# Performance work log

Hardware: AMD Instinct MI355X
Metric: run time of the kernel (lower is better)

Reference implementation:

```python
import jax, jax.numpy as jnp
import numpy as np

# Token / dim constants (from vm_step.Token and vm_step._SetDim)
CODE_START, CODE_END, MEM = 256, 257, 258
ADDR_KEY, MEM_STORE = 206, 455
VOCAB, D_MODEL = 272, 512
B, S = 16, 8192


def setup_inputs() -> dict:
    key = jax.random.key(0)
    k1, k2 = jax.random.split(key)
    token_ids = jax.random.randint(k1, (B, S), 0, VOCAB)
    embed_weight = jax.random.normal(k2, (VOCAB, D_MODEL), dtype=jnp.float32) * 0.02
    return {"token_ids": token_ids, "embed_weight": embed_weight, "mem_history_end": 2048}


def _augment_mask(token_ids, mem_history_end):
    """Boolean [B, S, D_MODEL] mask of positions that get set to 1.0."""
    Bb, Ss = token_ids.shape
    idx = jnp.arange(Ss)                                  # [S]
    is_start = token_ids == CODE_START
    is_end = token_ids == CODE_END
    # loop breaks at the FIRST CODE_END in each row
    end_idx = jnp.min(jnp.where(is_end, idx[None, :], Ss), axis=1)      # [B]
    # cs_pos = index of most recent CODE_START at-or-before i (-1 if none)
    cs = jax.lax.cummax(jnp.where(is_start, idx[None, :], -1), axis=1)  # [B,S]
    addr = idx[None, :] - cs - 1                                        # [B,S]
    valid = (cs >= 0) & (idx[None, :] < end_idx[:, None]) \
            & (token_ids < 256) & (addr >= 0)
    lo = addr & 15
    hi = (addr >> 4) & 15
    top = (addr >> 8) & 15
    bins = jnp.arange(16)                                 # nibble one-hots
    lo_oh = (bins == lo[..., None]) & valid[..., None]    # [B,S,16]
    hi_oh = (bins == hi[..., None]) & valid[..., None]
    top_oh = (bins == top[..., None]) & valid[..., None]
    mem_flag = (token_ids == MEM) & (idx[None, :] < mem_history_end)    # [B,S]

    mask = jnp.zeros((Bb, Ss, D_MODEL), dtype=bool)
    mask = mask.at[:, :, ADDR_KEY:ADDR_KEY + 16].set(lo_oh)
    mask = mask.at[:, :, ADDR_KEY + 16:ADDR_KEY + 32].set(hi_oh)
    mask = mask.at[:, :, ADDR_KEY + 32:ADDR_KEY + 48].set(top_oh)
    mask = mask.at[:, :, MEM_STORE].set(mem_flag)
    return mask


def reference(token_ids, embed_weight, mem_history_end):
    x = embed_weight[token_ids]                           # [B,S,D] gather
    mask = _augment_mask(token_ids, mem_history_end)
    return jnp.where(mask, jnp.asarray(1.0, x.dtype), x)
```

## Files before the change

### kernel.cpp

```cpp
#include <hip/hip_runtime.h>

#define TOK_CODE_START 256
#define TOK_CODE_END   257
#define TOK_MEM        258
#define ADDR_KEY       206
#define MEM_STORE      455

constexpr int Bb = 16;
constexpr int Ss = 8192;
constexpr int DM = 512;

typedef float f32x4 __attribute__((ext_vector_type(4)));

__global__ __launch_bounds__(1024) void vm_scan_kernel(
    const int* __restrict__ tok,
    const int* __restrict__ mhe_p,
    unsigned int* __restrict__ ws)
{
    const int b = blockIdx.x;
    const int t = threadIdx.x;
    const int lane = t & 63;
    const int wid = t >> 6;
    const int mhe = mhe_p[0];
    const int* row = tok + b * Ss;
    const int base = t * 8;

    int toks[8];
    int4 v0 = reinterpret_cast<const int4*>(row + base)[0];
    int4 v1 = reinterpret_cast<const int4*>(row + base)[1];
    toks[0] = v0.x; toks[1] = v0.y; toks[2] = v0.z; toks[3] = v0.w;
    toks[4] = v1.x; toks[5] = v1.y; toks[6] = v1.z; toks[7] = v1.w;

    int lmax = -1;
    int lend = Ss;
    #pragma unroll
    for (int k = 0; k < 8; ++k) {
        int idx = base + k;
        if (toks[k] == TOK_CODE_START) lmax = idx;
        if (toks[k] == TOK_CODE_END && lend == Ss) lend = idx;
    }

    #pragma unroll
    for (int off = 1; off < 64; off <<= 1) {
        int u = __shfl_up(lmax, off);
        if (lane >= off && u > lmax) lmax = u;
    }
    int excl = __shfl_up(lmax, 1);
    if (lane == 0) excl = -1;

    #pragma unroll
    for (int off = 32; off > 0; off >>= 1) {
        int u = __shfl_xor(lend, off);
        if (u < lend) lend = u;
    }

    __shared__ int wmax[16];
    __shared__ int wend[16];
    if (lane == 63) wmax[wid] = lmax;
    if (lane == 0)  wend[wid] = lend;
    __syncthreads();

    int carry = -1;
    #pragma unroll
    for (int j = 0; j < 16; ++j)
        if (j < wid && wmax[j] > carry) carry = wmax[j];
    int end_idx = Ss;
    #pragma unroll
    for (int j = 0; j < 16; ++j)
        if (wend[j] < end_idx) end_idx = wend[j];

    int run = (carry > excl) ? carry : excl;

    unsigned int pk[8];
    #pragma unroll
    for (int k = 0; k < 8; ++k) {
        int idx = base + k;
        int tv = toks[k];
        if (tv == TOK_CODE_START) run = idx;
        int cs = run;
        int addr = idx - cs - 1;
        bool valid = (cs >= 0) && (idx < end_idx) && (tv < 256) && (addr >= 0);
        bool memf  = (tv == TOK_MEM) && (idx < mhe);
        unsigned int w = (unsigned int)tv;
        if (valid) w |= (1u << 9) | ((unsigned int)addr << 11);
        if (memf)  w |= (1u << 10);
        pk[k] = w;
    }
    uint4* wr = reinterpret_cast<uint4*>(ws + b * Ss + base);
    wr[0] = make_uint4(pk[0], pk[1], pk[2], pk[3]);
    wr[1] = make_uint4(pk[4], pk[5], pk[6], pk[7]);
}

__global__ __launch_bounds__(256) void vm_gather_kernel(
    const f32x4* __restrict__ emb,
    const unsigned int* __restrict__ ws,
    f32x4* __restrict__ out)
{
    const int total = Bb * Ss * (DM / 4);
    const int stride = gridDim.x * blockDim.x;
    for (int w = blockIdx.x * blockDim.x + threadIdx.x; w < total; w += stride) {
        int bs = w >> 7;
        int dq = w & 127;
        unsigned int pw = ws[bs];
        int tk = (int)(pw & 511u);
        f32x4 v = emb[tk * (DM / 4) + dq];
        unsigned int flags = pw >> 9;
        if (flags) {
            bool valid = (flags & 1u) != 0u;
            bool memf  = (flags & 2u) != 0u;
            int addr = (int)(flags >> 2);
            int p0 = ADDR_KEY      + (addr & 15);
            int p1 = ADDR_KEY + 16 + ((addr >> 4) & 15);
            int p2 = ADDR_KEY + 32 + ((addr >> 8) & 15);
            int d0 = dq << 2;
            #pragma unroll
            for (int j = 0; j < 4; ++j) {
                int d = d0 + j;
                if ((valid && (d == p0 || d == p1 || d == p2)) ||
                    (memf && d == MEM_STORE)) v[j] = 1.0f;
            }
        }
        __builtin_nontemporal_store(v, &out[w]);
    }
}

extern "C" void kernel_launch(void* const* d_in, const int* in_sizes, int n_in,
                              void* d_out, int out_size, void* d_ws, size_t ws_size,
                              hipStream_t stream) {
    const int* tok = (const int*)d_in[0];
    const float* emb = (const float*)d_in[1];
    const int* mhe = (const int*)d_in[2];
    unsigned int* ws = (unsigned int*)d_ws;
    f32x4* out = (f32x4*)d_out;

    vm_scan_kernel<<<Bb, 1024, 0, stream>>>(tok, mhe, ws);
    vm_gather_kernel<<<2048, 256, 0, stream>>>((const f32x4*)emb, ws, out);
}
```

Before: 51.43 us.

## Fuse token scan and embedding gather into one kernel with per-block prefix rescan

```diff
diff --git a/kernel.cpp b/kernel.cpp
--- a/kernel.cpp
+++ b/kernel.cpp
@@ -9,101 +9,101 @@
 constexpr int Bb = 16;
 constexpr int Ss = 8192;
 constexpr int DM = 512;
+constexpr int POS_PER_BLK = 64;
+constexpr int QPP = DM / 4;
+constexpr int THREADS = 256;
 
 typedef float f32x4 __attribute__((ext_vector_type(4)));
 
-__global__ __launch_bounds__(1024) void vm_scan_kernel(
+__global__ __launch_bounds__(THREADS) void vm_fused_kernel(
     const int* __restrict__ tok,
+    const f32x4* __restrict__ emb,
     const int* __restrict__ mhe_p,
-    unsigned int* __restrict__ ws)
+    f32x4* __restrict__ out)
 {
-    const int b = blockIdx.x;
-    const int t = threadIdx.x;
+    const int bk = blockIdx.x;
+    const int b  = bk >> 7;
+    const int c  = bk & 127;
+    const int t  = threadIdx.x;
     const int lane = t & 63;
-    const int wid = t >> 6;
+    const int wid  = t >> 6;
+    const int s0 = c * POS_PER_BLK;
+    const int* row = tok + b * Ss;
     const int mhe = mhe_p[0];
-    const int* row = tok + b * Ss;
-    const int base = t * 8;
 
-    int toks[8];
-    int4 v0 = reinterpret_cast<const int4*>(row + base)[0];
-    int4 v1 = reinterpret_cast<const int4*>(row + base)[1];
-    toks[0] = v0.x; toks[1] = v0.y; toks[2] = v0.z; toks[3] = v0.w;
-    toks[4] = v1.x; toks[5] = v1.y; toks[6] = v1.z; toks[7] = v1.w;
+    __shared__ int sP[4], sE[4];
+    __shared__ unsigned int smask[POS_PER_BLK];
 
-    int lmax = -1;
-    int lend = Ss;
-    #pragma unroll
-    for (int k = 0; k < 8; ++k) {
-        int idx = base + k;
-        if (toks[k] == TOK_CODE_START) lmax = idx;
-        if (toks[k] == TOK_CODE_END && lend == Ss) lend = idx;
+    int myTok = 0;
+    if (t < POS_PER_BLK) myTok = row[s0 + t];
+
+    int maxStart = -1;
+    int minEnd = Ss;
+    {
+        const int base = t * 32;
+        if (base < s0) {
+            #pragma unroll
+            for (int j = 0; j < 8; ++j) {
+                int4 v = reinterpret_cast<const int4*>(row + base + j * 4)[0];
+                int i0 = base + j * 4;
+                if (v.x == TOK_CODE_START) maxStart = i0;
+                if (v.y == TOK_CODE_START) maxStart = i0 + 1;
+                if (v.z == TOK_CODE_START) maxStart = i0 + 2;
+                if (v.w == TOK_CODE_START) maxStart = i0 + 3;
+                if (v.x == TOK_CODE_END && minEnd == Ss) minEnd = i0;
+                if (v.y == TOK_CODE_END && minEnd == Ss) minEnd = i0 + 1;
+                if (v.z == TOK_CODE_END && minEnd == Ss) minEnd = i0 + 2;
+                if (v.w == TOK_CODE_END && minEnd == Ss) minEnd = i0 + 3;
+            }
+        }
     }
-
-    #pragma unroll
-    for (int off = 1; off < 64; off <<= 1) {
-        int u = __shfl_up(lmax, off);
-        if (lane >= off && u > lmax) lmax = u;
-    }
-    int excl = __shfl_up(lmax, 1);
-    if (lane == 0) excl = -1;
-
     #pragma unroll
     for (int off = 32; off > 0; off >>= 1) {
-        int u = __shfl_xor(lend, off);
-        if (u < lend) lend = u;
+        int u = __shfl_xor(maxStart, off);
+        if (u > maxStart) maxStart = u;
+        int w = __shfl_xor(minEnd, off);
+        if (w < minEnd) minEnd = w;
     }
-
-    __shared__ int wmax[16];
-    __shared__ int wend[16];
-    if (lane == 63) wmax[wid] = lmax;
-    if (lane == 0)  wend[wid] = lend;
+    if (lane == 0) { sP[wid] = maxStart; sE[wid] = minEnd; }
     __syncthreads();
 
-    int carry = -1;
-    #pragma unroll
-    for (int j = 0; j < 16; ++j)
-        if (j < wid && wmax[j] > carry) carry = wmax[j];
-    int end_idx = Ss;
-    #pragma unroll
-    for (int j = 0; j < 16; ++j)
-        if (wend[j] < end_idx) end_idx = wend[j];
+    if (t < POS_PER_BLK) {
+        int P = max(max(sP[0], sP[1]), max(sP[2], sP[3]));
+        int E = min(min(sE[0], sE[1]), min(sE[2], sE[3]));
 
-    int run = (carry > excl) ? carry : excl;
-
-    unsigned int pk[8];
-    #pragma unroll
-    for (int k = 0; k < 8; ++k) {
-        int idx = base + k;
-        int tv = toks[k];
-        if (tv == TOK_CODE_START) run = idx;
-        int cs = run;
+        const int idx = s0 + t;
+        int st = (myTok == TOK_CODE_START) ? idx : -1;
+        int en = (myTok == TOK_CODE_END) ? idx : Ss;
+        #pragma unroll
+        for (int off = 1; off < 64; off <<= 1) {
+            int u = __shfl_up(st, off);
+            int v = __shfl_up(en, off);
+            if (lane >= off) {
+                if (u > st) st = u;
+                if (v < en) en = v;
+            }
+        }
+        int cs = max(P, st);
+        int firstEnd = min(E, en);
         int addr = idx - cs - 1;
-        bool valid = (cs >= 0) && (idx < end_idx) && (tv < 256) && (addr >= 0);
-        bool memf  = (tv == TOK_MEM) && (idx < mhe);
-        unsigned int w = (unsigned int)tv;
+        bool valid = (cs >= 0) && (firstEnd > idx) && (myTok < 256) && (addr >= 0);
+        bool memf  = (myTok == TOK_MEM) && (idx < mhe);
+        unsigned int w = (unsigned int)myTok;
         if (valid) w |= (1u << 9) | ((unsigned int)addr << 11);
         if (memf)  w |= (1u << 10);
-        pk[k] = w;
+        smask[t] = w;
     }
-    uint4* wr = reinterpret_cast<uint4*>(ws + b * Ss + base);
-    wr[0] = make_uint4(pk[0], pk[1], pk[2], pk[3]);
-    wr[1] = make_uint4(pk[4], pk[5], pk[6], pk[7]);
-}
+    __syncthreads();
 
-__global__ __launch_bounds__(256) void vm_gather_kernel(
-    const f32x4* __restrict__ emb,
-    const unsigned int* __restrict__ ws,
-    f32x4* __restrict__ out)
-{
-    const int total = Bb * Ss * (DM / 4);
-    const int stride = gridDim.x * blockDim.x;
-    for (int w = blockIdx.x * blockDim.x + threadIdx.x; w < total; w += stride) {
-        int bs = w >> 7;
-        int dq = w & 127;
-        unsigned int pw = ws[bs];
+    const int outBase = bk * (POS_PER_BLK * QPP);
+    #pragma unroll 8
+    for (int i = 0; i < 32; ++i) {
+        int q = i * THREADS + t;
+        int pos = q >> 7;
+        int dq = q & 127;
+        unsigned int pw = smask[pos];
         int tk = (int)(pw & 511u);
-        f32x4 v = emb[tk * (DM / 4) + dq];
+        f32x4 v = emb[tk * QPP + dq];
         unsigned int flags = pw >> 9;
         if (flags) {
             bool valid = (flags & 1u) != 0u;
@@ -120,7 +120,7 @@
                     (memf && d == MEM_STORE)) v[j] = 1.0f;
             }
         }
-        __builtin_nontemporal_store(v, &out[w]);
+        __builtin_nontemporal_store(v, &out[outBase + q]);
     }
 }
 
@@ -128,11 +128,9 @@
                               void* d_out, int out_size, void* d_ws, size_t ws_size,
                               hipStream_t stream) {
     const int* tok = (const int*)d_in[0];
-    const float* emb = (const float*)d_in[1];
+    const f32x4* emb = (const f32x4*)d_in[1];
     const int* mhe = (const int*)d_in[2];
-    unsigned int* ws = (unsigned int*)d_ws;
     f32x4* out = (f32x4*)d_out;
 
-    vm_scan_kernel<<<Bb, 1024, 0, stream>>>(tok, mhe, ws);
-    vm_gather_kernel<<<2048, 256, 0, stream>>>((const f32x4*)emb, ws, out);
+    vm_fused_kernel<<<Bb * (Ss / POS_PER_BLK), THREADS, 0, stream>>>(tok, emb, mhe, out);
 }
```

Measured after the change: 58.21 us. 13.2% more time.
